# Kernel tuning notes

Hardware: AMD Instinct MI355X
Metric: run time of the kernel (lower is better)

Reference implementation:

```python
import jax, jax.numpy as jnp
import numpy as np
from jax import lax

CORR = 16  # corr_size in the original module


def _adaptive_pool16(x):
    # exact adaptive avg pool when H, W divisible by 16 (torch-equivalent)
    B, C, H, W = x.shape
    return x.reshape(B, C, CORR, H // CORR, CORR, W // CORR).mean(axis=(3, 5))


def _l2_normalize(x, eps=1e-12):
    # torch F.normalize default: L2 over dim=1, norm clamped to eps
    n = jnp.sqrt(jnp.sum(x * x, axis=1, keepdims=True))
    return x / jnp.maximum(n, eps)


def _instance_norm(x, eps=1e-5):
    # InstanceNorm2d, affine=False, biased variance over H,W per (b,c)
    mu = x.mean(axis=(2, 3), keepdims=True)
    var = jnp.mean((x - mu) ** 2, axis=(2, 3), keepdims=True)
    return (x - mu) * lax.rsqrt(var + eps)


def _corr_reduce(x, W1, b1, W2, b2):
    # 1x1 conv (256 -> fc) + bias
    y = jnp.einsum('bchw,oc->bohw', x, W1[:, :, 0, 0]) + b1[None, :, None, None]
    y = jax.nn.relu(_instance_norm(y))
    # 3x3 conv, padding=1, stride=1
    y = lax.conv_general_dilated(y, W2, (1, 1), 'SAME',
                                 dimension_numbers=('NCHW', 'OIHW', 'NCHW'))
    return y + b2[None, :, None, None]


def _corr(feat):
    # pooled [B,C,16,16] used as per-sample bank of 256 1x1 conv kernels
    pooled = _adaptive_pool16(feat)                      # [B,C,16,16]
    norm = _l2_normalize(feat)                           # [B,C,H,W]
    B, C = pooled.shape[:2]
    ker = pooled.reshape(B, C, CORR * CORR)              # [B,C,256]
    # corr[b,p,h,w] = sum_c ker[b,c,p] * norm[b,c,h,w]
    return jnp.einsum('bcp,bchw->bphw', ker, norm)


def setup_inputs() -> dict:
    key = jax.random.key(0)
    ks = jax.random.split(key, 6)
    B, C, H, W = 16, 256, 96, 96
    fc = 256
    return {
        'F_infrared': jax.random.normal(ks[0], (B, C, H, W), jnp.float32),
        'F_visible': jax.random.normal(ks[1], (B, C, H, W), jnp.float32),
        'W1': jax.random.normal(ks[2], (fc, CORR * CORR, 1, 1), jnp.float32) * 0.05,
        'b1': jax.random.normal(ks[3], (fc,), jnp.float32) * 0.05,
        'W2': jax.random.normal(ks[4], (fc, fc, 3, 3), jnp.float32) * 0.05,
        'b2': jax.random.normal(ks[5], (fc,), jnp.float32) * 0.05,
    }


def reference(F_infrared, F_visible, W1, b1, W2, b2):
    VIS_corr = _corr_reduce(_corr(F_visible), W1, b1, W2, b2)
    IR_corr = _corr_reduce(_corr(F_infrared), W1, b1, W2, b2)
    return (IR_corr, VIS_corr)
```

## Files before the change

kernel.cpp:

```cpp
#include <hip/hip_runtime.h>
#include <hip/hip_bf16.h>

#define BATCH 16
#define CH    256
#define HH    96
#define WW    96
#define HWSZ  9216
#define FCH   256
#define PP    256

typedef float f32x4 __attribute__((ext_vector_type(4)));
typedef short bf16x8 __attribute__((ext_vector_type(8)));
typedef unsigned short ushortT;

#define APAD_ELEMS 2458624
#define APAD_CHUNKS 307328

__device__ __forceinline__ void gload16(const void* g, void* l) {
    __builtin_amdgcn_global_load_lds((const __attribute__((address_space(1))) void*)g,
                                     (__attribute__((address_space(3))) void*)l, 16, 0, 0);
}
__device__ __forceinline__ float bfu2f(ushortT u) {
    return __uint_as_float(((unsigned)u) << 16);
}
__device__ __forceinline__ ushortT f2bfu(float f) {
    __hip_bfloat16 hb = __float2bfloat16(f);
    return *reinterpret_cast<ushortT*>(&hb);
}

__global__ void pool16_k(const float* __restrict__ feat, float* __restrict__ pooled)
{
    int bc = blockIdx.x;
    const float* src = feat + (size_t)bc * HWSZ;
    int t = threadIdx.x;
    int pr = t >> 4, pc = t & 15;
    float s = 0.f;
#pragma unroll
    for (int i = 0; i < 6; ++i)
#pragma unroll
        for (int j = 0; j < 6; ++j)
            s += src[(pr * 6 + i) * WW + pc * 6 + j];
    pooled[(size_t)bc * PP + t] = s * (1.0f / 36.0f);
}

__global__ void fpack_k(const float* __restrict__ feat, ushortT* __restrict__ fpack,
                        float* __restrict__ rnorm)
{
    int b = blockIdx.y;
    int hw = blockIdx.x * 256 + threadIdx.x;
    const float* src = feat + (size_t)b * CH * HWSZ + hw;
    uint4* dst = (uint4*)fpack + (size_t)b * 32 * HWSZ + hw;
    float ss = 0.f;
    for (int cb = 0; cb < 32; ++cb) {
        union { ushortT u[8]; uint4 v; } pk;
#pragma unroll
        for (int i = 0; i < 8; ++i) {
            float v = src[(size_t)(cb * 8 + i) * HWSZ];
            ss += v * v;
            pk.u[i] = f2bfu(v);
        }
        dst[(size_t)cb * HWSZ] = pk.v;
    }
    rnorm[b * HWSZ + hw] = 1.0f / fmaxf(sqrtf(ss), 1e-12f);
}

__global__ void gemmM_k(const float* __restrict__ W1, const float* __restrict__ pooled,
                        ushortT* __restrict__ Mb16)
{
    int b = blockIdx.z;
    int o0 = blockIdx.y * 16, c0 = blockIdx.x * 16;
    int ty = threadIdx.y, tx = threadIdx.x;
    __shared__ float Ws[16][17], Ps[16][17];
    float acc = 0.f;
    for (int p0 = 0; p0 < PP; p0 += 16) {
        Ws[ty][tx] = W1[(o0 + ty) * PP + p0 + tx];
        Ps[ty][tx] = pooled[((size_t)b * CH + (c0 + ty)) * PP + p0 + tx];
        __syncthreads();
#pragma unroll
        for (int p = 0; p < 16; ++p) acc += Ws[ty][p] * Ps[tx][p];
        __syncthreads();
    }
    int c = c0 + tx, o = o0 + ty;
    Mb16[(((size_t)b * 32 + (c >> 3)) * 256 + o) * 8 + (c & 7)] = f2bfu(acc);
}

__global__ void repack_w2_k(const float* __restrict__ W2, ushortT* __restrict__ W2r2)
{
    int e = blockIdx.x * 256 + threadIdx.x;
    int ci = e & 7, o = (e >> 3) & 255, cb = (e >> 11) & 31, s = e >> 16;
    int c = cb * 8 + ci;
    W2r2[e] = f2bfu(W2[((size_t)o * 256 + c) * 9 + s]);
}

__global__ void zero_k(uint4* __restrict__ p, size_t n)
{
    size_t i = (size_t)blockIdx.x * 256 + threadIdx.x;
    size_t stride = (size_t)gridDim.x * 256;
    uint4 z; z.x = 0; z.y = 0; z.z = 0; z.w = 0;
    for (; i < n; i += stride) p[i] = z;
}

__global__ __launch_bounds__(256, 4) void gemmYm_k(const ushortT* __restrict__ Mb16,
                                                   const ushortT* __restrict__ fpack,
                                                   const float* __restrict__ rnorm,
                                                   ushortT* __restrict__ apad, int b0)
{
    int bl = blockIdx.z, bg = b0 + bl;
    int hw0 = blockIdx.x * 128;
    int o0 = blockIdx.y * 128;
    int tid = threadIdx.x, wave = tid >> 6, lane = tid & 63;
    int wm = wave >> 1, wn = wave & 1;
    int lr = lane & 15, kb = lane >> 4;

    __shared__ __align__(16) char smem[34816];
    uint4* AsC = (uint4*)smem;
    uint4* BsC = AsC + 512;
    const bf16x8* AsV = (const bf16x8*)smem;
    const bf16x8* BsV = AsV + 512;
    ushortT* T = (ushortT*)smem;

    const uint4* MbC = (const uint4*)Mb16 + (size_t)bg * 32 * 256;
    const uint4* fpC = (const uint4*)fpack + (size_t)bg * 32 * HWSZ;

    f32x4 acc[4][4] = {};

    for (int cb0 = 0; cb0 < 32; cb0 += 4) {
#pragma unroll
        for (int i = 0; i < 2; ++i) {
            int e = tid + i * 256;
            int kk = e >> 7, j = e & 127;
            gload16(MbC + (size_t)(cb0 + kk) * 256 + o0 + j, AsC + e);
            gload16(fpC + (size_t)(cb0 + kk) * HWSZ + hw0 + j, BsC + e);
        }
        __syncthreads();
        bf16x8 af[4], bfv[4];
#pragma unroll
        for (int mf = 0; mf < 4; ++mf) af[mf] = AsV[kb * 128 + wm * 64 + mf * 16 + lr];
#pragma unroll
        for (int nf = 0; nf < 4; ++nf) bfv[nf] = BsV[kb * 128 + wn * 64 + nf * 16 + lr];
#pragma unroll
        for (int mf = 0; mf < 4; ++mf)
#pragma unroll
            for (int nf = 0; nf < 4; ++nf)
                acc[mf][nf] = __builtin_amdgcn_mfma_f32_16x16x32_bf16(af[mf], bfv[nf], acc[mf][nf], 0, 0, 0);
        __syncthreads();
    }

    float rn[4];
#pragma unroll
    for (int nf = 0; nf < 4; ++nf)
        rn[nf] = rnorm[(size_t)bg * HWSZ + hw0 + wn * 64 + nf * 16 + lr];

#pragma unroll
    for (int mf = 0; mf < 4; ++mf)
#pragma unroll
        for (int nf = 0; nf < 4; ++nf)
#pragma unroll
            for (int r = 0; r < 4; ++r)
                T[(wn * 64 + nf * 16 + lr) * 136 + wm * 64 + mf * 16 + kb * 4 + r] =
                    f2bfu(acc[mf][nf][r] * rn[nf]);
    __syncthreads();

    uint4* apC = (uint4*)apad + (size_t)bl * APAD_CHUNKS;
    int ob0 = blockIdx.y * 16;
#pragma unroll
    for (int i = 0; i < 8; ++i) {
        int e = tid + i * 256;
        int hw_l = e >> 4, ob = e & 15;
        uint4 v = *(uint4*)&T[hw_l * 136 + ob * 8];
        int hw = hw0 + hw_l;
        int h = hw / 96, w = hw - h * 96;
        apC[(size_t)((h + 1) * 32 + ob0 + ob) * 98 + (w + 1)] = v;
    }
}

__global__ void instats2_k(const ushortT* __restrict__ apad, float* __restrict__ mu,
                           float* __restrict__ istd)
{
    int ob = blockIdx.x, bl = blockIdx.y;
    const uint4* apC = (const uint4*)apad + (size_t)bl * APAD_CHUNKS;
    float s[8] = {}, s2[8] = {};
    for (int e = threadIdx.x; e < HWSZ; e += 256) {
        int row = e / 96;
        int w = e - row * 96;
        uint4 v = apC[(size_t)((row + 1) * 32 + ob) * 98 + w + 1];
        const ushortT* u = (const ushortT*)&v;
#pragma unroll
        for (int k = 0; k < 8; ++k) {
            float f = bfu2f(u[k]);
            s[k] += f; s2[k] += f * f;
        }
    }
#pragma unroll
    for (int off = 32; off > 0; off >>= 1) {
#pragma unroll
        for (int k = 0; k < 8; ++k) {
            s[k]  += __shfl_down(s[k],  off, 64);
            s2[k] += __shfl_down(s2[k], off, 64);
        }
    }
    __shared__ float sh[4][16];
    int wid = threadIdx.x >> 6;
    if ((threadIdx.x & 63) == 0) {
#pragma unroll
        for (int k = 0; k < 8; ++k) { sh[wid][k] = s[k]; sh[wid][8 + k] = s2[k]; }
    }
    __syncthreads();
    if (threadIdx.x < 8) {
        int k = threadIdx.x;
        float S  = sh[0][k] + sh[1][k] + sh[2][k] + sh[3][k];
        float S2 = sh[0][8 + k] + sh[1][8 + k] + sh[2][8 + k] + sh[3][8 + k];
        float m   = S * (1.0f / HWSZ);
        float var = S2 * (1.0f / HWSZ) - m * m;
        if (var < 0.f) var = 0.f;
        mu[bl * 256 + ob * 8 + k]   = m;
        istd[bl * 256 + ob * 8 + k] = rsqrtf(var + 1e-5f);
    }
}

__global__ void nr_k(ushortT* __restrict__ apad, const float* __restrict__ mu,
                     const float* __restrict__ istd)
{
    int row = blockIdx.x + 1, bl = blockIdx.y;
    __shared__ float smu[256], sis[256];
    smu[threadIdx.x] = mu[bl * 256 + threadIdx.x];
    sis[threadIdx.x] = istd[bl * 256 + threadIdx.x];
    __syncthreads();
    uint4* apC = (uint4*)apad + (size_t)bl * APAD_CHUNKS + (size_t)row * 32 * 98;
    for (int e = threadIdx.x; e < 3072; e += 256) {
        int ob = e / 96;
        int w = e - ob * 96 + 1;
        uint4 v = apC[(size_t)ob * 98 + w];
        ushortT* u = (ushortT*)&v;
#pragma unroll
        for (int k = 0; k < 8; ++k) {
            float f = (bfu2f(u[k]) - smu[ob * 8 + k]) * sis[ob * 8 + k];
            u[k] = f2bfu(f > 0.f ? f : 0.f);
        }
        apC[(size_t)ob * 98 + w] = v;
    }
}

__global__ __launch_bounds__(256, 4) void conv3m2_k(const ushortT* __restrict__ apad,
                                                    const ushortT* __restrict__ W2r2,
                                                    const float* __restrict__ b2,
                                                    float* __restrict__ out)
{
    int h0 = blockIdx.x * 2;
    int o0 = blockIdx.y * 64;
    int bl = blockIdx.z;
    int tid = threadIdx.x;
    int wave = tid >> 6, lane = tid & 63;
    int wr = wave >> 1, wh = wave & 1;
    int lr = lane & 15, kb = lane >> 4;

    __shared__ __align__(16) ushortT As[768 * 8];
    __shared__ __align__(16) ushortT Bs[1024 * 8];

    const uint4* apadC = (const uint4*)apad + (size_t)bl * APAD_CHUNKS;
    const uint4* w2C   = (const uint4*)W2r2;
    uint4* AsC = (uint4*)As;
    uint4* BsC = (uint4*)Bs;
    const bf16x8* AsV = (const bf16x8*)As;
    const bf16x8* BsV = (const bf16x8*)Bs;

    f32x4 acc[4][3] = {};

    for (int kh = 0; kh < 3; ++kh) {
        for (int c0 = 0; c0 < 256; c0 += 32) {
            int cb0 = c0 >> 3;
#pragma unroll
            for (int i = 0; i < 3; ++i) {
                int e = tid + i * 256;
                int o = e & 63, kk = (e >> 6) & 3, kw = e >> 8;
                gload16(w2C + (size_t)((kh * 3 + kw) * 32 + cb0 + kk) * 256 + o0 + o, AsC + e);
            }
#pragma unroll
            for (int i = 0; i < 4; ++i) {
                int e = tid + i * 256;
                int se = e < 784 ? e : 783;
                int w = se % 98, r = se / 98;
                int rr = r >> 2, kk = r & 3;
                gload16(apadC + (size_t)((h0 + kh + rr) * 32 + cb0 + kk) * 98 + w, BsC + e);
            }
            __syncthreads();
#pragma unroll
            for (int kw = 0; kw < 3; ++kw) {
                bf16x8 af[4];
#pragma unroll
                for (int mf = 0; mf < 4; ++mf)
                    af[mf] = AsV[(kw * 4 + kb) * 64 + mf * 16 + lr];
#pragma unroll
                for (int nf = 0; nf < 3; ++nf) {
                    bf16x8 bfr = BsV[(wr * 4 + kb) * 98 + wh * 48 + nf * 16 + lr + kw];
#pragma unroll
                    for (int mf = 0; mf < 4; ++mf)
                        acc[mf][nf] = __builtin_amdgcn_mfma_f32_16x16x32_bf16(af[mf], bfr, acc[mf][nf], 0, 0, 0);
                }
            }
            __syncthreads();
        }
    }

    int h = h0 + wr;
    float* obase = out + (size_t)bl * FCH * HWSZ + (size_t)h * WW + wh * 48;
#pragma unroll
    for (int mf = 0; mf < 4; ++mf) {
#pragma unroll
        for (int r = 0; r < 4; ++r) {
            int o = o0 + mf * 16 + kb * 4 + r;
            float bias = b2[o];
            float* orow = obase + (size_t)o * HWSZ;
#pragma unroll
            for (int nf = 0; nf < 3; ++nf)
                orow[nf * 16 + lr] = acc[mf][nf][r] + bias;
        }
    }
}

extern "C" void kernel_launch(void* const* d_in, const int* in_sizes, int n_in,
                              void* d_out, int out_size, void* d_ws, size_t ws_size,
                              hipStream_t stream)
{
    const float* Fir  = (const float*)d_in[0];
    const float* Fvis = (const float*)d_in[1];
    const float* W1   = (const float*)d_in[2];
    const float* W2   = (const float*)d_in[4];
    const float* b2   = (const float*)d_in[5];
    float* out = (float*)d_out;

    char* w = (char*)d_ws;
    const size_t poolB = (size_t)BATCH * CH * PP * 4;
    const size_t MbB   = (size_t)BATCH * 32 * 256 * 8 * 2;
    const size_t rnB   = (size_t)BATCH * HWSZ * 4;
    const size_t stB   = (size_t)BATCH * FCH * 4;
    const size_t w2rB  = (size_t)9 * 32 * 256 * 8 * 2;
    const size_t fpB   = (size_t)BATCH * 32 * HWSZ * 8 * 2;

    size_t off = 0;
    float*   pooled = (float*)(w + off);   off += poolB;
    ushortT* Mb16   = (ushortT*)(w + off); off += MbB;
    float*   rnorm  = (float*)(w + off);   off += rnB;
    float*   mu     = (float*)(w + off);   off += stB;
    float*   istd   = (float*)(w + off);   off += stB;
    ushortT* W2r2   = (ushortT*)(w + off); off += w2rB;
    ushortT* fpack  = (ushortT*)(w + off); off += fpB;
    const size_t fixed = off;

    const size_t apadB = (size_t)APAD_ELEMS * 2;
    size_t avail = ws_size > fixed ? ws_size - fixed : 0;
    int NB = (int)(avail / apadB);
    if (NB > BATCH) NB = BATCH;
    if (NB < 1) NB = 1;
    ushortT* apad = (ushortT*)(w + fixed);

    repack_w2_k<<<2304, 256, 0, stream>>>(W2, W2r2);
    zero_k<<<2048, 256, 0, stream>>>((uint4*)apad, (size_t)NB * APAD_CHUNKS);

    for (int f = 0; f < 2; ++f) {
        const float* feat = (f == 0) ? Fir : Fvis;
        float* o_ = out + (size_t)f * BATCH * FCH * HWSZ;

        fpack_k<<<dim3(36, BATCH), 256, 0, stream>>>(feat, fpack, rnorm);
        pool16_k<<<BATCH * CH, 256, 0, stream>>>(feat, pooled);
        gemmM_k<<<dim3(16, 16, BATCH), dim3(16, 16), 0, stream>>>(W1, pooled, Mb16);

        for (int b0 = 0; b0 < BATCH; b0 += NB) {
            int nb = BATCH - b0 < NB ? BATCH - b0 : NB;
            gemmYm_k<<<dim3(72, 2, nb), 256, 0, stream>>>(Mb16, fpack, rnorm, apad, b0);
            instats2_k<<<dim3(32, nb), 256, 0, stream>>>(apad, mu, istd);
            nr_k<<<dim3(96, nb), 256, 0, stream>>>(apad, mu, istd);
            conv3m2_k<<<dim3(48, 4, nb), 256, 0, stream>>>(apad, W2r2, b2,
                                                           o_ + (size_t)b0 * FCH * HWSZ);
        }
    }
}
```

Measured before the change: 719.7 us.

## Double-buffer GEMM and conv LDS tiles, pool from packed bf16, zero only borders

Adds two-stage LDS double buffering to the gemmYm and 3x3 conv kernels, so the next K-slice's global-to-LDS loads are issued before the current slice's MFMAs. This removes one barrier per iteration. The conv kernel's launch bound drops to 2 blocks per CU to make room for the doubled LDS. Pooling now reads the packed bf16 feature tensor instead of the fp32 input, which cuts read traffic but pools bf16-rounded values. The apad buffer now has only its padding border zeroed instead of being fully cleared, and the transpose staging stride changes from 136 to 130.

```diff
diff --git a/kernel.cpp b/kernel.cpp
--- a/kernel.cpp
+++ b/kernel.cpp
@@ -28,21 +28,6 @@
     return *reinterpret_cast<ushortT*>(&hb);
 }
 
-__global__ void pool16_k(const float* __restrict__ feat, float* __restrict__ pooled)
-{
-    int bc = blockIdx.x;
-    const float* src = feat + (size_t)bc * HWSZ;
-    int t = threadIdx.x;
-    int pr = t >> 4, pc = t & 15;
-    float s = 0.f;
-#pragma unroll
-    for (int i = 0; i < 6; ++i)
-#pragma unroll
-        for (int j = 0; j < 6; ++j)
-            s += src[(pr * 6 + i) * WW + pc * 6 + j];
-    pooled[(size_t)bc * PP + t] = s * (1.0f / 36.0f);
-}
-
 __global__ void fpack_k(const float* __restrict__ feat, ushortT* __restrict__ fpack,
                         float* __restrict__ rnorm)
 {
@@ -62,6 +47,28 @@
         dst[(size_t)cb * HWSZ] = pk.v;
     }
     rnorm[b * HWSZ + hw] = 1.0f / fmaxf(sqrtf(ss), 1e-12f);
+}
+
+__global__ void pool16b_k(const ushortT* __restrict__ fpack, float* __restrict__ pooled)
+{
+    int cb = blockIdx.x, b = blockIdx.y;
+    const uint4* fp = (const uint4*)fpack + ((size_t)b * 32 + cb) * HWSZ;
+    int t = threadIdx.x;
+    int pr = t >> 4, pc = t & 15;
+    float s[8] = {};
+#pragma unroll
+    for (int i = 0; i < 6; ++i) {
+#pragma unroll
+        for (int j = 0; j < 6; ++j) {
+            uint4 v = fp[(pr * 6 + i) * WW + pc * 6 + j];
+            const ushortT* u = (const ushortT*)&v;
+#pragma unroll
+            for (int k = 0; k < 8; ++k) s[k] += bfu2f(u[k]);
+        }
+    }
+#pragma unroll
+    for (int k = 0; k < 8; ++k)
+        pooled[((size_t)b * CH + cb * 8 + k) * PP + t] = s[k] * (1.0f / 36.0f);
 }
 
 __global__ void gemmM_k(const float* __restrict__ W1, const float* __restrict__ pooled,
@@ -92,12 +99,21 @@
     W2r2[e] = f2bfu(W2[((size_t)o * 256 + c) * 9 + s]);
 }
 
-__global__ void zero_k(uint4* __restrict__ p, size_t n)
-{
-    size_t i = (size_t)blockIdx.x * 256 + threadIdx.x;
-    size_t stride = (size_t)gridDim.x * 256;
+__global__ void zborder_k(uint4* __restrict__ apad)
+{
+    int bl = blockIdx.x;
+    uint4* apC = apad + (size_t)bl * APAD_CHUNKS;
     uint4 z; z.x = 0; z.y = 0; z.z = 0; z.w = 0;
-    for (; i < n; i += stride) p[i] = z;
+    for (int e = threadIdx.x; e < 3136; e += 256) {
+        apC[e] = z;
+        apC[(size_t)97 * 32 * 98 + e] = z;
+    }
+    for (int e = threadIdx.x; e < 3072; e += 256) {
+        int row = 1 + (e >> 5), cb = e & 31;
+        size_t base = (size_t)(row * 32 + cb) * 98;
+        apC[base] = z;
+        apC[base + 97] = z;
+    }
 }
 
 __global__ __launch_bounds__(256, 4) void gemmYm_k(const ushortT* __restrict__ Mb16,
@@ -112,27 +128,33 @@
     int wm = wave >> 1, wn = wave & 1;
     int lr = lane & 15, kb = lane >> 4;
 
-    __shared__ __align__(16) char smem[34816];
-    uint4* AsC = (uint4*)smem;
-    uint4* BsC = AsC + 512;
-    const bf16x8* AsV = (const bf16x8*)smem;
-    const bf16x8* BsV = AsV + 512;
-    ushortT* T = (ushortT*)smem;
+    __shared__ __align__(16) char smem[33280];
 
     const uint4* MbC = (const uint4*)Mb16 + (size_t)bg * 32 * 256;
     const uint4* fpC = (const uint4*)fpack + (size_t)bg * 32 * HWSZ;
 
     f32x4 acc[4][4] = {};
 
-    for (int cb0 = 0; cb0 < 32; cb0 += 4) {
+    auto STAGE = [&](int buf, int s) {
+        int cb0 = s * 4;
+        uint4* A = (uint4*)smem + (size_t)buf * 1024;
+        uint4* B = A + 512;
 #pragma unroll
         for (int i = 0; i < 2; ++i) {
             int e = tid + i * 256;
             int kk = e >> 7, j = e & 127;
-            gload16(MbC + (size_t)(cb0 + kk) * 256 + o0 + j, AsC + e);
-            gload16(fpC + (size_t)(cb0 + kk) * HWSZ + hw0 + j, BsC + e);
-        }
+            gload16(MbC + (size_t)(cb0 + kk) * 256 + o0 + j, A + e);
+            gload16(fpC + (size_t)(cb0 + kk) * HWSZ + hw0 + j, B + e);
+        }
+    };
+
+    STAGE(0, 0);
+    for (int s = 0; s < 8; ++s) {
+        int buf = s & 1;
         __syncthreads();
+        if (s < 7) STAGE(buf ^ 1, s + 1);
+        const bf16x8* AsV = (const bf16x8*)(smem + (size_t)buf * 16384);
+        const bf16x8* BsV = AsV + 512;
         bf16x8 af[4], bfv[4];
 #pragma unroll
         for (int mf = 0; mf < 4; ++mf) af[mf] = AsV[kb * 128 + wm * 64 + mf * 16 + lr];
@@ -143,21 +165,22 @@
 #pragma unroll
             for (int nf = 0; nf < 4; ++nf)
                 acc[mf][nf] = __builtin_amdgcn_mfma_f32_16x16x32_bf16(af[mf], bfv[nf], acc[mf][nf], 0, 0, 0);
-        __syncthreads();
-    }
+    }
+    __syncthreads();
 
     float rn[4];
 #pragma unroll
     for (int nf = 0; nf < 4; ++nf)
         rn[nf] = rnorm[(size_t)bg * HWSZ + hw0 + wn * 64 + nf * 16 + lr];
 
+    ushortT* T = (ushortT*)smem;
 #pragma unroll
     for (int mf = 0; mf < 4; ++mf)
 #pragma unroll
         for (int nf = 0; nf < 4; ++nf)
 #pragma unroll
             for (int r = 0; r < 4; ++r)
-                T[(wn * 64 + nf * 16 + lr) * 136 + wm * 64 + mf * 16 + kb * 4 + r] =
+                T[(wn * 64 + nf * 16 + lr) * 130 + wm * 64 + mf * 16 + kb * 4 + r] =
                     f2bfu(acc[mf][nf][r] * rn[nf]);
     __syncthreads();
 
@@ -167,7 +190,7 @@
     for (int i = 0; i < 8; ++i) {
         int e = tid + i * 256;
         int hw_l = e >> 4, ob = e & 15;
-        uint4 v = *(uint4*)&T[hw_l * 136 + ob * 8];
+        uint4 v = *(uint4*)&T[hw_l * 130 + ob * 8];
         int hw = hw0 + hw_l;
         int h = hw / 96, w = hw - h * 96;
         apC[(size_t)((h + 1) * 32 + ob0 + ob) * 98 + (w + 1)] = v;
@@ -241,7 +264,7 @@
     }
 }
 
-__global__ __launch_bounds__(256, 4) void conv3m2_k(const ushortT* __restrict__ apad,
+__global__ __launch_bounds__(256, 2) void conv3m3_k(const ushortT* __restrict__ apad,
                                                     const ushortT* __restrict__ W2r2,
                                                     const float* __restrict__ b2,
                                                     float* __restrict__ out)
@@ -254,51 +277,54 @@
     int wr = wave >> 1, wh = wave & 1;
     int lr = lane & 15, kb = lane >> 4;
 
-    __shared__ __align__(16) ushortT As[768 * 8];
-    __shared__ __align__(16) ushortT Bs[1024 * 8];
+    __shared__ __align__(16) uint4 AsC[2][768];
+    __shared__ __align__(16) uint4 BsC[2][1024];
 
     const uint4* apadC = (const uint4*)apad + (size_t)bl * APAD_CHUNKS;
     const uint4* w2C   = (const uint4*)W2r2;
-    uint4* AsC = (uint4*)As;
-    uint4* BsC = (uint4*)Bs;
-    const bf16x8* AsV = (const bf16x8*)As;
-    const bf16x8* BsV = (const bf16x8*)Bs;
 
     f32x4 acc[4][3] = {};
 
-    for (int kh = 0; kh < 3; ++kh) {
-        for (int c0 = 0; c0 < 256; c0 += 32) {
-            int cb0 = c0 >> 3;
-#pragma unroll
-            for (int i = 0; i < 3; ++i) {
-                int e = tid + i * 256;
-                int o = e & 63, kk = (e >> 6) & 3, kw = e >> 8;
-                gload16(w2C + (size_t)((kh * 3 + kw) * 32 + cb0 + kk) * 256 + o0 + o, AsC + e);
+    auto STAGE = [&](int buf, int it) {
+        int kh = it >> 3, cb0 = (it & 7) << 2;
+#pragma unroll
+        for (int i = 0; i < 3; ++i) {
+            int e = tid + i * 256;
+            int o = e & 63, kk = (e >> 6) & 3, kw = e >> 8;
+            gload16(w2C + (size_t)((kh * 3 + kw) * 32 + cb0 + kk) * 256 + o0 + o,
+                    &AsC[buf][e]);
+        }
+#pragma unroll
+        for (int i = 0; i < 4; ++i) {
+            int e = tid + i * 256;
+            int se = e < 784 ? e : 783;
+            int w = se % 98, r = se / 98;
+            int rr = r >> 2, kk = r & 3;
+            gload16(apadC + (size_t)((h0 + kh + rr) * 32 + cb0 + kk) * 98 + w,
+                    &BsC[buf][e]);
+        }
+    };
+
+    STAGE(0, 0);
+    for (int it = 0; it < 24; ++it) {
+        int buf = it & 1;
+        __syncthreads();
+        if (it < 23) STAGE(buf ^ 1, it + 1);
+        const bf16x8* AsV = (const bf16x8*)&AsC[buf][0];
+        const bf16x8* BsV = (const bf16x8*)&BsC[buf][0];
+#pragma unroll
+        for (int kw = 0; kw < 3; ++kw) {
+            bf16x8 af[4];
+#pragma unroll
+            for (int mf = 0; mf < 4; ++mf)
+                af[mf] = AsV[(kw * 4 + kb) * 64 + mf * 16 + lr];
+#pragma unroll
+            for (int nf = 0; nf < 3; ++nf) {
+                bf16x8 bfr = BsV[(wr * 4 + kb) * 98 + wh * 48 + nf * 16 + lr + kw];
+#pragma unroll
+                for (int mf = 0; mf < 4; ++mf)
+                    acc[mf][nf] = __builtin_amdgcn_mfma_f32_16x16x32_bf16(af[mf], bfr, acc[mf][nf], 0, 0, 0);
             }
-#pragma unroll
-            for (int i = 0; i < 4; ++i) {
-                int e = tid + i * 256;
-                int se = e < 784 ? e : 783;
-                int w = se % 98, r = se / 98;
-                int rr = r >> 2, kk = r & 3;
-                gload16(apadC + (size_t)((h0 + kh + rr) * 32 + cb0 + kk) * 98 + w, BsC + e);
-            }
-            __syncthreads();
-#pragma unroll
-            for (int kw = 0; kw < 3; ++kw) {
-                bf16x8 af[4];
-#pragma unroll
-                for (int mf = 0; mf < 4; ++mf)
-                    af[mf] = AsV[(kw * 4 + kb) * 64 + mf * 16 + lr];
-#pragma unroll
-                for (int nf = 0; nf < 3; ++nf) {
-                    bf16x8 bfr = BsV[(wr * 4 + kb) * 98 + wh * 48 + nf * 16 + lr + kw];
-#pragma unroll
-                    for (int mf = 0; mf < 4; ++mf)
-                        acc[mf][nf] = __builtin_amdgcn_mfma_f32_16x16x32_bf16(af[mf], bfr, acc[mf][nf], 0, 0, 0);
-                }
-            }
-            __syncthreads();
         }
     }
 
@@ -355,14 +381,14 @@
     ushortT* apad = (ushortT*)(w + fixed);
 
     repack_w2_k<<<2304, 256, 0, stream>>>(W2, W2r2);
-    zero_k<<<2048, 256, 0, stream>>>((uint4*)apad, (size_t)NB * APAD_CHUNKS);
+    zborder_k<<<NB, 256, 0, stream>>>((uint4*)apad);
 
     for (int f = 0; f < 2; ++f) {
         const float* feat = (f == 0) ? Fir : Fvis;
         float* o_ = out + (size_t)f * BATCH * FCH * HWSZ;
 
         fpack_k<<<dim3(36, BATCH), 256, 0, stream>>>(feat, fpack, rnorm);
-        pool16_k<<<BATCH * CH, 256, 0, stream>>>(feat, pooled);
+        pool16b_k<<<dim3(32, BATCH), 256, 0, stream>>>(fpack, pooled);
         gemmM_k<<<dim3(16, 16, BATCH), dim3(16, 16), 0, stream>>>(W1, pooled, Mb16);
 
         for (int b0 = 0; b0 < BATCH; b0 += NB) {
@@ -370,7 +396,7 @@
             gemmYm_k<<<dim3(72, 2, nb), 256, 0, stream>>>(Mb16, fpack, rnorm, apad, b0);
             instats2_k<<<dim3(32, nb), 256, 0, stream>>>(apad, mu, istd);
             nr_k<<<dim3(96, nb), 256, 0, stream>>>(apad, mu, istd);
-            conv3m2_k<<<dim3(48, 4, nb), 256, 0, stream>>>(apad, W2r2, b2,
+            conv3m3_k<<<dim3(48, 4, nb), 256, 0, stream>>>(apad, W2r2, b2,
                                                            o_ + (size_t)b0 * FCH * HWSZ);
         }
     }
```

New measurement: 773.8 us. 7.5% more time.
